# Kernel optimization log

Measured on AMD Instinct MI355X. Metric: run time of the kernel, lower is better.

The kernel has to match this reference:

```python
import jax, jax.numpy as jnp
import numpy as np

NEG_SLOPE = 0.2
EPS = 1e-16

N_NODES = 50000
N_EDGES = 800000
IN_C = 256
HID_C = 64
HEADS = 4
OUT_C = 128
N_GRAPHS = 100


def setup_inputs() -> dict:
    key = jax.random.key(0)
    ks = jax.random.split(key, 12)
    x = jax.random.normal(ks[0], (N_NODES, IN_C), dtype=jnp.float32)
    edge_index = jax.random.randint(ks[1], (2, N_EDGES), 0, N_NODES, dtype=jnp.int64)
    batch = jnp.sort(jax.random.randint(ks[2], (N_NODES,), 0, N_GRAPHS, dtype=jnp.int64))
    s1 = 1.0 / np.sqrt(IN_C)
    s2 = 1.0 / np.sqrt(HEADS * HID_C)
    W1 = jax.random.uniform(ks[3], (IN_C, HEADS * HID_C), jnp.float32, -s1, s1)
    att_src1 = jax.random.uniform(ks[4], (HEADS, HID_C), jnp.float32, -s1, s1)
    att_dst1 = jax.random.uniform(ks[5], (HEADS, HID_C), jnp.float32, -s1, s1)
    bias1 = jnp.zeros((HEADS * HID_C,), jnp.float32)
    W2 = jax.random.uniform(ks[6], (HEADS * HID_C, OUT_C), jnp.float32, -s2, s2)
    att_src2 = jax.random.uniform(ks[7], (1, OUT_C), jnp.float32, -s2, s2)
    att_dst2 = jax.random.uniform(ks[8], (1, OUT_C), jnp.float32, -s2, s2)
    bias2 = jnp.zeros((OUT_C,), jnp.float32)
    return {"x": x, "W1": W1, "att_src1": att_src1, "att_dst1": att_dst1,
            "bias1": bias1, "W2": W2, "att_src2": att_src2, "att_dst2": att_dst2,
            "bias2": bias2, "edge_index": edge_index, "batch": batch,
            "num_graphs": N_GRAPHS}


def gat_conv(x, W, att_src, att_dst, bias, src, dst, heads, ch):
    # x: [N, F_in]; W: [F_in, heads*ch]; att_*: [heads, ch]
    n = x.shape[0]
    h = (x @ W).reshape(n, heads, ch)                      # [N, H, C]
    a_src = jnp.sum(h * att_src[None], axis=-1)            # [N, H]
    a_dst = jnp.sum(h * att_dst[None], axis=-1)            # [N, H]
    alpha = a_src[src] + a_dst[dst]                        # [E, H]
    alpha = jax.nn.leaky_relu(alpha, NEG_SLOPE)
    # segment softmax over destination nodes (every node has a self-loop)
    amax = jax.ops.segment_max(alpha, dst, num_segments=n)
    e = jnp.exp(alpha - amax[dst])
    denom = jax.ops.segment_sum(e, dst, num_segments=n)
    alpha = e / (denom[dst] + EPS)                         # [E, H]
    msg = h[src] * alpha[:, :, None]                       # [E, H, C]
    out = jax.ops.segment_sum(msg, dst, num_segments=n)    # [N, H, C]
    return out.reshape(n, heads * ch) + bias


def reference(x, W1, att_src1, att_dst1, bias1, W2, att_src2, att_dst2, bias2,
              edge_index, batch, num_graphs):
    n = x.shape[0]
    loops = jnp.arange(n, dtype=edge_index.dtype)
    src = jnp.concatenate([edge_index[0], loops])
    dst = jnp.concatenate([edge_index[1], loops])
    h = gat_conv(x, W1, att_src1, att_dst1, bias1, src, dst, HEADS, HID_C)
    h = jax.nn.relu(h)
    h = gat_conv(h, W2, att_src2, att_dst2, bias2, src, dst, 1, OUT_C)
    h = jax.nn.relu(h)
    # global mean pool over graphs
    sums = jax.ops.segment_sum(h, batch, num_segments=num_graphs)
    cnt = jax.ops.segment_sum(jnp.ones((n, 1), h.dtype), batch, num_segments=num_graphs)
    return sums / jnp.maximum(cnt, 1.0)
```

## Files before the change

kernel.cpp:

```cpp
#include <hip/hip_runtime.h>
#include <hip/hip_bf16.h>
#include <hip/hip_fp16.h>

#define N_NODES 50000
#define N_EDGES 800000
#define E_TOT   (N_EDGES + N_NODES)
#define IN_C    256
#define H1C     256
#define HEADS   4
#define HID_C   64
#define OUT_C   128
#define N_GRAPHS 100
#define NEG_SLOPE 0.2f
#define EPS_F 1e-16f
#define SCAN_BLOCKS 196

#define NBUCKET 391
#define SORT_BLOCKS 104
#define EDGES_PER_SB 8192
#define BH_STRIDE 392
#define STAGE_CAP 3072

#define PREP_CAST_BLOCKS   12500
#define PREP_W1_BLOCKS     256
#define PREP_W2_BLOCKS     128
#define PREP_HIST_BLOCKS   3321
#define PREP_BOUNDS_BLOCKS 196
#define PREP_DOUT_BLOCKS   50
#define PREP_TOTAL (PREP_CAST_BLOCKS + PREP_W1_BLOCKS + PREP_W2_BLOCKS + PREP_HIST_BLOCKS + PREP_BOUNDS_BLOCKS + PREP_DOUT_BLOCKS)

typedef _Float16 half8_t __attribute__((ext_vector_type(8)));
typedef float f32x4 __attribute__((ext_vector_type(4)));

__global__ __launch_bounds__(256) void prep_kernel(const float* __restrict__ x,
                                                   _Float16* __restrict__ xh,
                                                   const float* __restrict__ W1,
                                                   _Float16* __restrict__ W1t,
                                                   const float* __restrict__ W2,
                                                   _Float16* __restrict__ W2t,
                                                   const int* __restrict__ ei,
                                                   int* __restrict__ hist,
                                                   const int* __restrict__ batch,
                                                   int* __restrict__ gstart,
                                                   float* __restrict__ d_out) {
    int b = blockIdx.x;
    int tid = threadIdx.x;
    if (b < PREP_CAST_BLOCKS) {
        int idx = b * 256 + tid;
        float4 v = reinterpret_cast<const float4*>(x)[idx];
        union { _Float16 h[4]; uint2 u; } p;
        p.h[0] = (_Float16)v.x; p.h[1] = (_Float16)v.y;
        p.h[2] = (_Float16)v.z; p.h[3] = (_Float16)v.w;
        reinterpret_cast<uint2*>(xh)[idx] = p.u;
        return;
    }
    b -= PREP_CAST_BLOCKS;
    if (b < PREP_W1_BLOCKS) {
        int idx = b * 256 + tid;
        int n = idx >> 8, k = idx & 255;
        W1t[idx] = (_Float16)W1[k * 256 + n];
        return;
    }
    b -= PREP_W1_BLOCKS;
    if (b < PREP_W2_BLOCKS) {
        int idx = b * 256 + tid;
        int n = idx >> 8, k = idx & 255;
        W2t[idx] = (_Float16)W2[k * 128 + n];
        return;
    }
    b -= PREP_W2_BLOCKS;
    if (b < PREP_HIST_BLOCKS) {
        int idx = b * 256 + tid;
        if (idx < N_EDGES) {
            int d = ei[N_EDGES + idx];
            if (d >= 0 && d < N_NODES) atomicAdd(&hist[d], 1);
        } else if (idx < E_TOT) {
            atomicAdd(&hist[idx - N_EDGES], 1);
        }
        return;
    }
    b -= PREP_HIST_BLOCKS;
    if (b < PREP_BOUNDS_BLOCKS) {
        int idx = b * 256 + tid;
        if (idx >= N_NODES) return;
        int g = batch[idx];
        if (g < 0) g = 0; if (g >= N_GRAPHS) g = N_GRAPHS - 1;
        if (idx == 0) {
            for (int j = 0; j <= g; ++j) gstart[j] = 0;
        } else {
            int gp = batch[idx - 1];
            if (gp < 0) gp = 0; if (gp >= N_GRAPHS) gp = N_GRAPHS - 1;
            for (int j = gp + 1; j <= g; ++j) gstart[j] = idx;
        }
        if (idx == N_NODES - 1) {
            for (int j = g + 1; j <= N_GRAPHS; ++j) gstart[j] = N_NODES;
        }
        return;
    }
    b -= PREP_BOUNDS_BLOCKS;
    {
        int idx = b * 256 + tid;
        if (idx < N_GRAPHS * 128) d_out[idx] = 0.f;
    }
}

__global__ __launch_bounds__(256) void scan_phase1(const int* __restrict__ hist,
                                                   int* __restrict__ blockSums) {
    __shared__ int lds[256];
    int idx = blockIdx.x * 256 + threadIdx.x;
    int v = (idx < N_NODES) ? hist[idx] : 0;
    lds[threadIdx.x] = v;
    __syncthreads();
#pragma unroll
    for (int off = 128; off > 0; off >>= 1) {
        if (threadIdx.x < off) lds[threadIdx.x] += lds[threadIdx.x + off];
        __syncthreads();
    }
    if (threadIdx.x == 0) blockSums[blockIdx.x] = lds[0];
}

__global__ __launch_bounds__(256) void scan_phase3(const int* __restrict__ hist,
                                                   const int* __restrict__ blockSums,
                                                   int* __restrict__ row_ptr) {
    __shared__ int lds[256];
    __shared__ int s_off;
    int b = blockIdx.x;
    int t = threadIdx.x;
    if (t < 64) {
        int acc = 0;
        for (int i = t; i < b; i += 64) acc += blockSums[i];
#pragma unroll
        for (int off = 32; off > 0; off >>= 1) acc += __shfl_down(acc, off);
        if (t == 0) s_off = acc;
    }
    int idx = b * 256 + t;
    int v = (idx < N_NODES) ? hist[idx] : 0;
    lds[t] = v;
    __syncthreads();
#pragma unroll
    for (int off = 1; off < 256; off <<= 1) {
        int u = (t >= off) ? lds[t - off] : 0;
        __syncthreads();
        lds[t] += u;
        __syncthreads();
    }
    int excl = lds[t] - v + s_off;
    if (idx < N_NODES) row_ptr[idx] = excl;
    if (idx == N_NODES - 1) row_ptr[N_NODES] = excl + v;
}

__global__ __launch_bounds__(256) void bucket_hist(const int* __restrict__ ei,
                                                   int* __restrict__ bhist) {
    __shared__ int bh[NBUCKET];
    int tid = threadIdx.x;
    for (int t = tid; t < NBUCKET; t += 256) bh[t] = 0;
    __syncthreads();
    int base = blockIdx.x * EDGES_PER_SB;
#pragma unroll 4
    for (int k = 0; k < EDGES_PER_SB / 256; ++k) {
        int idx = base + k * 256 + tid;
        int d = -1;
        if (idx < N_EDGES) d = ei[N_EDGES + idx];
        else if (idx < E_TOT) d = idx - N_EDGES;
        if (d >= 0 && d < N_NODES) atomicAdd(&bh[d >> 7], 1);
    }
    __syncthreads();
    for (int t = tid; t < NBUCKET; t += 256)
        bhist[blockIdx.x * BH_STRIDE + t] = bh[t];
}

__global__ __launch_bounds__(64) void bucket_scan(int* __restrict__ bhist) {
    int j = blockIdx.x;
    int lane = threadIdx.x;
    int carry = 0;
    for (int b0 = 0; b0 < SORT_BLOCKS; b0 += 64) {
        int b = b0 + lane;
        int v = (b < SORT_BLOCKS) ? bhist[b * BH_STRIDE + j] : 0;
        int inc = v;
#pragma unroll
        for (int off = 1; off < 64; off <<= 1) {
            int u = __shfl_up(inc, off);
            if (lane >= off) inc += u;
        }
        if (b < SORT_BLOCKS) bhist[b * BH_STRIDE + j] = inc - v + carry;
        carry += __shfl(inc, 63);
    }
}

__global__ __launch_bounds__(256) void bucket_bin(const int* __restrict__ ei,
                                                  const int* __restrict__ row_ptr,
                                                  const int* __restrict__ bhist,
                                                  int* __restrict__ ebuf) {
    __shared__ int cur[NBUCKET];
    int tid = threadIdx.x;
    for (int t = tid; t < NBUCKET; t += 256)
        cur[t] = row_ptr[t << 7] + bhist[blockIdx.x * BH_STRIDE + t];
    __syncthreads();
    int base = blockIdx.x * EDGES_PER_SB;
#pragma unroll 4
    for (int k = 0; k < EDGES_PER_SB / 256; ++k) {
        int idx = base + k * 256 + tid;
        int s = 0, d = -1;
        if (idx < N_EDGES) { s = ei[idx]; d = ei[N_EDGES + idx]; }
        else if (idx < E_TOT) { s = idx - N_EDGES; d = s; }
        if (d >= 0 && d < N_NODES) {
            int p = atomicAdd(&cur[d >> 7], 1);
            ebuf[p] = (s & 0xFFFF) | ((d & 127) << 16);
        }
    }
}

__global__ __launch_bounds__(256) void bucket_sort(const int* __restrict__ row_ptr,
                                                   const int* __restrict__ ebuf,
                                                   int* __restrict__ ssrc) {
    __shared__ int cur2[128];
    __shared__ int stage[STAGE_CAP];
    int j = blockIdx.x;
    int tid = threadIdx.x;
    int jn0 = j << 7;
    int nEnd = jn0 + 128; if (nEnd > N_NODES) nEnd = N_NODES;
    int lo = row_ptr[jn0];
    int hi = row_ptr[nEnd];
    int span = hi - lo;
    if (tid < nEnd - jn0) cur2[tid] = row_ptr[jn0 + tid] - lo;
    __syncthreads();
    if (span <= STAGE_CAP) {
        for (int t = lo + tid; t < hi; t += 256) {
            int v = ebuf[t];
            int p = atomicAdd(&cur2[v >> 16], 1);
            stage[p] = v & 0xFFFF;
        }
        __syncthreads();
        for (int t = tid; t < span; t += 256) ssrc[lo + t] = stage[t];
    } else {
        for (int t = lo + tid; t < hi; t += 256) {
            int v = ebuf[t];
            int p = atomicAdd(&cur2[v >> 16], 1);
            ssrc[lo + p] = v & 0xFFFF;
        }
    }
}

__global__ __launch_bounds__(256) void gemm_mfma_kernel(const _Float16* __restrict__ A,
                                                        const _Float16* __restrict__ Bt,
                                                        _Float16* __restrict__ C,
                                                        int mode,
                                                        const float* __restrict__ attS,
                                                        const float* __restrict__ attD,
                                                        float* __restrict__ a_src_o,
                                                        float* __restrict__ a_dst_o,
                                                        int M, int N) {
    __shared__ _Float16 As[128][48];
    __shared__ _Float16 Bs[128][48];
    __shared__ float lds_ps[128];
    __shared__ float lds_pd[128];
    const int tid = threadIdx.x;
    const int tileM = blockIdx.x * 128;
    const int tileN = blockIdx.y * 128;
    const int w = tid >> 6, lane = tid & 63;
    const int wm = (w >> 1) * 64, wn = (w & 1) * 64;
    const int quad = lane >> 4, mlane = lane & 15;
    const int srow = tid >> 2;
    const int schunk = (tid & 3) * 8;

    f32x4 zero = {0.f, 0.f, 0.f, 0.f};
    f32x4 acc[4][4];
#pragma unroll
    for (int i = 0; i < 4; ++i)
#pragma unroll
        for (int j = 0; j < 4; ++j) acc[i][j] = zero;

    const uint4* Av = reinterpret_cast<const uint4*>(A);
    const uint4* Bv = reinterpret_cast<const uint4*>(Bt);
    const int r0 = tileM + srow, r1 = r0 + 64;
    const bool ok0 = r0 < M, ok1 = r1 < M;
    const int bn0 = tileN + srow, bn1 = bn0 + 64;
    const uint4 z4 = make_uint4(0, 0, 0, 0);

    for (int k0 = 0; k0 < 256; k0 += 32) {
        const int kc = (k0 >> 3) + (tid & 3);
        uint4 a0 = ok0 ? Av[(size_t)r0 * 32 + kc] : z4;
        uint4 a1 = ok1 ? Av[(size_t)r1 * 32 + kc] : z4;
        uint4 b0 = Bv[(size_t)bn0 * 32 + kc];
        uint4 b1 = Bv[(size_t)bn1 * 32 + kc];
        __syncthreads();
        *reinterpret_cast<uint4*>(&As[srow][schunk]) = a0;
        *reinterpret_cast<uint4*>(&As[srow + 64][schunk]) = a1;
        *reinterpret_cast<uint4*>(&Bs[srow][schunk]) = b0;
        *reinterpret_cast<uint4*>(&Bs[srow + 64][schunk]) = b1;
        __syncthreads();
        half8_t af[4], bf[4];
#pragma unroll
        for (int mt = 0; mt < 4; ++mt)
            af[mt] = *reinterpret_cast<const half8_t*>(&As[wm + mt * 16 + mlane][quad * 8]);
#pragma unroll
        for (int nt = 0; nt < 4; ++nt)
            bf[nt] = *reinterpret_cast<const half8_t*>(&Bs[wn + nt * 16 + mlane][quad * 8]);
#pragma unroll
        for (int mt = 0; mt < 4; ++mt)
#pragma unroll
            for (int nt = 0; nt < 4; ++nt)
                acc[mt][nt] = __builtin_amdgcn_mfma_f32_16x16x32_f16(af[mt], bf[nt], acc[mt][nt], 0, 0, 0);
    }
#pragma unroll
    for (int mt = 0; mt < 4; ++mt) {
#pragma unroll
        for (int i = 0; i < 4; ++i) {
            int row = tileM + wm + mt * 16 + quad * 4 + i;
            if (row < M) {
                _Float16* cp = C + (size_t)row * N + tileN + wn;
#pragma unroll
                for (int nt = 0; nt < 4; ++nt)
                    cp[nt * 16 + mlane] = (_Float16)acc[mt][nt][i];
            }
        }
    }
    if (mode == 1) {
        int hd = (tileN + wn) >> 6;
        float as[4], ad[4];
#pragma unroll
        for (int nt = 0; nt < 4; ++nt) {
            as[nt] = attS[hd * 64 + nt * 16 + mlane];
            ad[nt] = attD[hd * 64 + nt * 16 + mlane];
        }
#pragma unroll
        for (int mt = 0; mt < 4; ++mt) {
#pragma unroll
            for (int i = 0; i < 4; ++i) {
                float ps = acc[mt][0][i] * as[0] + acc[mt][1][i] * as[1]
                         + acc[mt][2][i] * as[2] + acc[mt][3][i] * as[3];
                float pd = acc[mt][0][i] * ad[0] + acc[mt][1][i] * ad[1]
                         + acc[mt][2][i] * ad[2] + acc[mt][3][i] * ad[3];
#pragma unroll
                for (int off = 1; off < 16; off <<= 1) {
                    ps += __shfl_xor(ps, off);
                    pd += __shfl_xor(pd, off);
                }
                if (mlane == 0) {
                    int row = tileM + wm + mt * 16 + quad * 4 + i;
                    if (row < M) {
                        a_src_o[row * 4 + hd] = ps;
                        a_dst_o[row * 4 + hd] = pd;
                    }
                }
            }
        }
    } else if (mode == 2) {
        float as[4], ad[4];
#pragma unroll
        for (int nt = 0; nt < 4; ++nt) {
            as[nt] = attS[wn + nt * 16 + mlane];
            ad[nt] = attD[wn + nt * 16 + mlane];
        }
        float psa[4][4], pda[4][4];
#pragma unroll
        for (int mt = 0; mt < 4; ++mt) {
#pragma unroll
            for (int i = 0; i < 4; ++i) {
                float ps = acc[mt][0][i] * as[0] + acc[mt][1][i] * as[1]
                         + acc[mt][2][i] * as[2] + acc[mt][3][i] * as[3];
                float pd = acc[mt][0][i] * ad[0] + acc[mt][1][i] * ad[1]
                         + acc[mt][2][i] * ad[2] + acc[mt][3][i] * ad[3];
#pragma unroll
                for (int off = 1; off < 16; off <<= 1) {
                    ps += __shfl_xor(ps, off);
                    pd += __shfl_xor(pd, off);
                }
                psa[mt][i] = ps; pda[mt][i] = pd;
            }
        }
        __syncthreads();
        if (wn == 0 && mlane == 0) {
#pragma unroll
            for (int mt = 0; mt < 4; ++mt)
#pragma unroll
                for (int i = 0; i < 4; ++i) {
                    int lr = wm + mt * 16 + quad * 4 + i;
                    lds_ps[lr] = psa[mt][i];
                    lds_pd[lr] = pda[mt][i];
                }
        }
        __syncthreads();
        if (wn == 64 && mlane == 0) {
#pragma unroll
            for (int mt = 0; mt < 4; ++mt)
#pragma unroll
                for (int i = 0; i < 4; ++i) {
                    int lr = wm + mt * 16 + quad * 4 + i;
                    int row = tileM + lr;
                    if (row < M) {
                        a_src_o[row] = psa[mt][i] + lds_ps[lr];
                        a_dst_o[row] = pda[mt][i] + lds_pd[lr];
                    }
                }
        }
    }
}

__device__ __forceinline__ float lrelu(float x) { return x > 0.f ? x : NEG_SLOPE * x; }

__global__ __launch_bounds__(256) void edge1_kernel(const int* __restrict__ row_ptr,
                                                    const int* __restrict__ ssrc,
                                                    const __half* __restrict__ h1h,
                                                    const float* __restrict__ a_src,
                                                    const float* __restrict__ a_dst,
                                                    const float* __restrict__ bias,
                                                    __half* __restrict__ out) {
    int node = blockIdx.x * 4 + (threadIdx.x >> 6);
    int lane = threadIdx.x & 63;
    int hf   = lane >> 5;
    int cl   = lane & 31;
    int hd   = cl >> 3;
    int start = row_ptr[node], end = row_ptr[node + 1];
    int em1 = end - 1;
    float adh = a_dst[node * 4 + hd];

    const uint4* h1v = reinterpret_cast<const uint4*>(h1h);
    float4 aA0 = make_float4(0.f,0.f,0.f,0.f), aA1 = make_float4(0.f,0.f,0.f,0.f);
    float4 aB0 = make_float4(0.f,0.f,0.f,0.f), aB1 = make_float4(0.f,0.f,0.f,0.f);
    float s = 0.f;
    for (int e = start; e < end; e += 4) {
        int e0 = e + hf;
        int e1 = e + 2 + hf;
        int i0 = ssrc[e0 <= em1 ? e0 : em1];
        int i1 = ssrc[e1 <= em1 ? e1 : em1];
        float r0 = a_src[i0 * 4 + hd];
        float r1 = a_src[i1 * 4 + hd];
        uint4 q0 = h1v[(size_t)i0 * 32 + cl];
        uint4 q1 = h1v[(size_t)i1 * 32 + cl];
        float w0 = (e0 < end) ? __expf(lrelu(r0 + adh)) : 0.f;
        float w1 = (e1 < end) ? __expf(lrelu(r1 + adh)) : 0.f;
        s += w0 + w1;
        float2 f;
        f = __half22float2(*reinterpret_cast<const __half2*>(&q0.x)); aA0.x += w0*f.x; aA0.y += w0*f.y;
        f = __half22float2(*reinterpret_cast<const __half2*>(&q0.y)); aA0.z += w0*f.x; aA0.w += w0*f.y;
        f = __half22float2(*reinterpret_cast<const __half2*>(&q0.z)); aA1.x += w0*f.x; aA1.y += w0*f.y;
        f = __half22float2(*reinterpret_cast<const __half2*>(&q0.w)); aA1.z += w0*f.x; aA1.w += w0*f.y;
        f = __half22float2(*reinterpret_cast<const __half2*>(&q1.x)); aB0.x += w1*f.x; aB0.y += w1*f.y;
        f = __half22float2(*reinterpret_cast<const __half2*>(&q1.y)); aB0.z += w1*f.x; aB0.w += w1*f.y;
        f = __half22float2(*reinterpret_cast<const __half2*>(&q1.z)); aB1.x += w1*f.x; aB1.y += w1*f.y;
        f = __half22float2(*reinterpret_cast<const __half2*>(&q1.w)); aB1.z += w1*f.x; aB1.w += w1*f.y;
    }
    float4 c0, c1;
    c0.x = aA0.x + aB0.x; c0.y = aA0.y + aB0.y; c0.z = aA0.z + aB0.z; c0.w = aA0.w + aB0.w;
    c1.x = aA1.x + aB1.x; c1.y = aA1.y + aB1.y; c1.z = aA1.z + aB1.z; c1.w = aA1.w + aB1.w;
    c0.x += __shfl_xor(c0.x, 32); c0.y += __shfl_xor(c0.y, 32);
    c0.z += __shfl_xor(c0.z, 32); c0.w += __shfl_xor(c0.w, 32);
    c1.x += __shfl_xor(c1.x, 32); c1.y += __shfl_xor(c1.y, 32);
    c1.z += __shfl_xor(c1.z, 32); c1.w += __shfl_xor(c1.w, 32);
    s += __shfl_xor(s, 32);
    float inv = 1.0f / (s + EPS_F);
    if (lane < 32) {
        const float4* b4 = reinterpret_cast<const float4*>(bias);
        float4 b0 = b4[cl * 2], b1 = b4[cl * 2 + 1];
        union { _Float16 h[8]; uint4 u; } st;
        st.h[0] = (_Float16)fmaxf(c0.x * inv + b0.x, 0.f);
        st.h[1] = (_Float16)fmaxf(c0.y * inv + b0.y, 0.f);
        st.h[2] = (_Float16)fmaxf(c0.z * inv + b0.z, 0.f);
        st.h[3] = (_Float16)fmaxf(c0.w * inv + b0.w, 0.f);
        st.h[4] = (_Float16)fmaxf(c1.x * inv + b1.x, 0.f);
        st.h[5] = (_Float16)fmaxf(c1.y * inv + b1.y, 0.f);
        st.h[6] = (_Float16)fmaxf(c1.z * inv + b1.z, 0.f);
        st.h[7] = (_Float16)fmaxf(c1.w * inv + b1.w, 0.f);
        reinterpret_cast<uint4*>(out)[(size_t)node * 32 + cl] = st.u;
    }
}

__global__ __launch_bounds__(256) void edge2_kernel(const int* __restrict__ row_ptr,
                                                    const int* __restrict__ ssrc,
                                                    const __half* __restrict__ h2h,
                                                    const float* __restrict__ a_src,
                                                    const float* __restrict__ a_dst,
                                                    const float* __restrict__ bias,
                                                    float* __restrict__ out) {
    int lane = threadIdx.x & 63;
    int node = blockIdx.x * 8 + ((threadIdx.x >> 6) << 1) + (lane >> 5);
    int sub  = (lane >> 4) & 1;
    int cl   = lane & 15;
    int start = row_ptr[node], end = row_ptr[node + 1];
    int em1 = end - 1;
    float ad = a_dst[node];

    const uint4* h2v = reinterpret_cast<const uint4*>(h2h);
    float4 aA0 = make_float4(0.f,0.f,0.f,0.f), aA1 = make_float4(0.f,0.f,0.f,0.f);
    float4 aB0 = make_float4(0.f,0.f,0.f,0.f), aB1 = make_float4(0.f,0.f,0.f,0.f);
    float s = 0.f;
    for (int e = start; e < end; e += 4) {
        int e0 = e + sub;
        int e1 = e + 2 + sub;
        int i0 = ssrc[e0 <= em1 ? e0 : em1];
        int i1 = ssrc[e1 <= em1 ? e1 : em1];
        float r0 = a_src[i0];
        float r1 = a_src[i1];
        uint4 q0 = h2v[(size_t)i0 * 16 + cl];
        uint4 q1 = h2v[(size_t)i1 * 16 + cl];
        float w0 = (e0 < end) ? __expf(lrelu(r0 + ad)) : 0.f;
        float w1 = (e1 < end) ? __expf(lrelu(r1 + ad)) : 0.f;
        s += w0 + w1;
        float2 f;
        f = __half22float2(*reinterpret_cast<const __half2*>(&q0.x)); aA0.x += w0*f.x; aA0.y += w0*f.y;
        f = __half22float2(*reinterpret_cast<const __half2*>(&q0.y)); aA0.z += w0*f.x; aA0.w += w0*f.y;
        f = __half22float2(*reinterpret_cast<const __half2*>(&q0.z)); aA1.x += w0*f.x; aA1.y += w0*f.y;
        f = __half22float2(*reinterpret_cast<const __half2*>(&q0.w)); aA1.z += w0*f.x; aA1.w += w0*f.y;
        f = __half22float2(*reinterpret_cast<const __half2*>(&q1.x)); aB0.x += w1*f.x; aB0.y += w1*f.y;
        f = __half22float2(*reinterpret_cast<const __half2*>(&q1.y)); aB0.z += w1*f.x; aB0.w += w1*f.y;
        f = __half22float2(*reinterpret_cast<const __half2*>(&q1.z)); aB1.x += w1*f.x; aB1.y += w1*f.y;
        f = __half22float2(*reinterpret_cast<const __half2*>(&q1.w)); aB1.z += w1*f.x; aB1.w += w1*f.y;
    }
    float4 c0, c1;
    c0.x = aA0.x + aB0.x; c0.y = aA0.y + aB0.y; c0.z = aA0.z + aB0.z; c0.w = aA0.w + aB0.w;
    c1.x = aA1.x + aB1.x; c1.y = aA1.y + aB1.y; c1.z = aA1.z + aB1.z; c1.w = aA1.w + aB1.w;
    c0.x += __shfl_xor(c0.x, 16); c0.y += __shfl_xor(c0.y, 16);
    c0.z += __shfl_xor(c0.z, 16); c0.w += __shfl_xor(c0.w, 16);
    c1.x += __shfl_xor(c1.x, 16); c1.y += __shfl_xor(c1.y, 16);
    c1.z += __shfl_xor(c1.z, 16); c1.w += __shfl_xor(c1.w, 16);
    s += __shfl_xor(s, 16);
    float inv = 1.0f / (s + EPS_F);
    if (sub == 0) {
        const float4* b4 = reinterpret_cast<const float4*>(bias);
        float4 b0 = b4[cl * 2], b1 = b4[cl * 2 + 1];
        float4 o0, o1;
        o0.x = fmaxf(c0.x * inv + b0.x, 0.f);
        o0.y = fmaxf(c0.y * inv + b0.y, 0.f);
        o0.z = fmaxf(c0.z * inv + b0.z, 0.f);
        o0.w = fmaxf(c0.w * inv + b0.w, 0.f);
        o1.x = fmaxf(c1.x * inv + b1.x, 0.f);
        o1.y = fmaxf(c1.y * inv + b1.y, 0.f);
        o1.z = fmaxf(c1.z * inv + b1.z, 0.f);
        o1.w = fmaxf(c1.w * inv + b1.w, 0.f);
        float4* o4 = reinterpret_cast<float4*>(out) + (size_t)node * 32 + cl * 2;
        o4[0] = o0;
        o4[1] = o1;
    }
}

#define POOL_CHUNK 64
__global__ __launch_bounds__(128) void pool_kernel(const float* __restrict__ out2,
                                                   const int* __restrict__ batch,
                                                   const int* __restrict__ gstart,
                                                   float* __restrict__ d_out) {
    int c = threadIdx.x;
    int node0 = blockIdx.x * POOL_CHUNK;
    int nodeEnd = node0 + POOL_CHUNK; if (nodeEnd > N_NODES) nodeEnd = N_NODES;
    if (node0 >= N_NODES) return;
    int gprev = batch[node0];
    float acc = 0.f;
    for (int node = node0; node < nodeEnd; ++node) {
        int g = batch[node];
        if (g != gprev) {
            if (gprev >= 0 && gprev < N_GRAPHS) {
                float cnt = (float)(gstart[gprev + 1] - gstart[gprev]);
                if (cnt < 1.f) cnt = 1.f;
                atomicAdd(&d_out[gprev * 128 + c], acc / cnt);
            }
            acc = 0.f;
            gprev = g;
        }
        acc += out2[(size_t)node * 128 + c];
    }
    if (gprev >= 0 && gprev < N_GRAPHS) {
        float cnt = (float)(gstart[gprev + 1] - gstart[gprev]);
        if (cnt < 1.f) cnt = 1.f;
        atomicAdd(&d_out[gprev * 128 + c], acc / cnt);
    }
}

extern "C" void kernel_launch(void* const* d_in, const int* in_sizes, int n_in,
                              void* d_out_v, int out_size, void* d_ws, size_t ws_size,
                              hipStream_t stream) {
    const float* x      = (const float*)d_in[0];
    const float* W1     = (const float*)d_in[1];
    const float* att_s1 = (const float*)d_in[2];
    const float* att_d1 = (const float*)d_in[3];
    const float* bias1  = (const float*)d_in[4];
    const float* W2     = (const float*)d_in[5];
    const float* att_s2 = (const float*)d_in[6];
    const float* att_d2 = (const float*)d_in[7];
    const float* bias2  = (const float*)d_in[8];
    const int*   ei     = (const int*)d_in[9];
    const int*   batch  = (const int*)d_in[10];
    float* d_out = (float*)d_out_v;

    float* ws = (float*)d_ws;
    _Float16* xh    = (_Float16*)ws;
    _Float16* h1h   = (_Float16*)(ws + 6400000);
    _Float16* out1h = (_Float16*)(ws + 12800000);
    _Float16* h2h   = (_Float16*)ws;
    float*    out2  = ws + 6400000;
    float* a_src1 = ws + 19200000;
    float* a_dst1 = a_src1 + 200000;
    float* a_src2 = a_dst1 + 200000;
    float* a_dst2 = a_src2 + 50000;
    int* hist     = (int*)(a_dst2 + 50000);
    int* row_ptr  = hist + 50000;
    int* ssrc     = row_ptr + 50016;
    int* ebuf     = ssrc + 850000;
    int* bhist    = ebuf + 851968;
    int* gstart   = bhist + (SORT_BLOCKS * BH_STRIDE);
    int* blockSums = gstart + 128;
    _Float16* W1t = (_Float16*)(blockSums + 256);
    _Float16* W2t = W1t + 65536;

    hipMemsetAsync(hist, 0, N_NODES * sizeof(int), stream);

    prep_kernel<<<PREP_TOTAL, 256, 0, stream>>>(x, xh, W1, W1t, W2, W2t,
                                                ei, hist, batch, gstart, d_out);

    scan_phase1<<<SCAN_BLOCKS, 256, 0, stream>>>(hist, blockSums);
    scan_phase3<<<SCAN_BLOCKS, 256, 0, stream>>>(hist, blockSums, row_ptr);

    bucket_hist<<<SORT_BLOCKS, 256, 0, stream>>>(ei, bhist);
    bucket_scan<<<NBUCKET, 64, 0, stream>>>(bhist);
    bucket_bin<<<SORT_BLOCKS, 256, 0, stream>>>(ei, row_ptr, bhist, ebuf);
    bucket_sort<<<NBUCKET, 256, 0, stream>>>(row_ptr, ebuf, ssrc);

    {
        dim3 g((N_NODES + 127) / 128, H1C / 128);
        gemm_mfma_kernel<<<g, 256, 0, stream>>>(xh, W1t, h1h, 1,
                                                att_s1, att_d1, a_src1, a_dst1,
                                                N_NODES, H1C);
    }
    edge1_kernel<<<N_NODES / 4, 256, 0, stream>>>(row_ptr, ssrc, (const __half*)h1h,
                                                  a_src1, a_dst1, bias1, (__half*)out1h);

    {
        dim3 g((N_NODES + 127) / 128, OUT_C / 128);
        gemm_mfma_kernel<<<g, 256, 0, stream>>>(out1h, W2t, h2h, 2,
                                                att_s2, att_d2, a_src2, a_dst2,
                                                N_NODES, OUT_C);
    }
    edge2_kernel<<<N_NODES / 8, 256, 0, stream>>>(row_ptr, ssrc, (const __half*)h2h,
                                                  a_src2, a_dst2, bias2, out2);

    pool_kernel<<<(N_NODES + POOL_CHUNK - 1) / POOL_CHUNK, 128, 0, stream>>>(out2, batch, gstart, d_out);
}
```

Baseline: 345.6 us.

## Software-pipeline neighbor gathers in GAT aggregation and repad GEMM LDS tiles

Both aggregation kernels now prefetch the next group's feature rows and attention scalars, and the index after that, one iteration ahead. This lets gather latency overlap with the current accumulation instead of serialising index, then feature loads, then math. The GEMM LDS tile row stride grows from 48 to 56 halves to change the bank-conflict pattern. The prefetch adds register pressure and an extra index load per iteration, and the new padding raises LDS use per block.

```diff
diff --git a/kernel.cpp b/kernel.cpp
--- a/kernel.cpp
+++ b/kernel.cpp
@@ -250,8 +250,8 @@
                                                         float* __restrict__ a_src_o,
                                                         float* __restrict__ a_dst_o,
                                                         int M, int N) {
-    __shared__ _Float16 As[128][48];
-    __shared__ _Float16 Bs[128][48];
+    __shared__ _Float16 As[128][56];
+    __shared__ _Float16 Bs[128][56];
     __shared__ float lds_ps[128];
     __shared__ float lds_pd[128];
     const int tid = threadIdx.x;
@@ -419,17 +419,31 @@
     float4 aA0 = make_float4(0.f,0.f,0.f,0.f), aA1 = make_float4(0.f,0.f,0.f,0.f);
     float4 aB0 = make_float4(0.f,0.f,0.f,0.f), aB1 = make_float4(0.f,0.f,0.f,0.f);
     float s = 0.f;
+
+    int e0 = start + hf, e1 = start + 2 + hf;
+    int i0 = ssrc[e0 <= em1 ? e0 : em1];
+    int i1 = ssrc[e1 <= em1 ? e1 : em1];
+    uint4 q0 = h1v[(size_t)i0 * 32 + cl];
+    uint4 q1 = h1v[(size_t)i1 * 32 + cl];
+    float r0 = a_src[i0 * 4 + hd];
+    float r1 = a_src[i1 * 4 + hd];
+    int f0 = start + 4 + hf, f1 = start + 6 + hf;
+    int j0 = ssrc[f0 <= em1 ? f0 : em1];
+    int j1 = ssrc[f1 <= em1 ? f1 : em1];
+
     for (int e = start; e < end; e += 4) {
-        int e0 = e + hf;
-        int e1 = e + 2 + hf;
-        int i0 = ssrc[e0 <= em1 ? e0 : em1];
-        int i1 = ssrc[e1 <= em1 ? e1 : em1];
-        float r0 = a_src[i0 * 4 + hd];
-        float r1 = a_src[i1 * 4 + hd];
-        uint4 q0 = h1v[(size_t)i0 * 32 + cl];
-        uint4 q1 = h1v[(size_t)i1 * 32 + cl];
-        float w0 = (e0 < end) ? __expf(lrelu(r0 + adh)) : 0.f;
-        float w1 = (e1 < end) ? __expf(lrelu(r1 + adh)) : 0.f;
+        uint4 p0, p1; float t0, t1;
+        if (e + 4 < end) {
+            p0 = h1v[(size_t)j0 * 32 + cl];
+            p1 = h1v[(size_t)j1 * 32 + cl];
+            t0 = a_src[j0 * 4 + hd];
+            t1 = a_src[j1 * 4 + hd];
+        }
+        int g0 = e + 8 + hf, g1 = e + 10 + hf;
+        int k0 = ssrc[g0 <= em1 ? g0 : em1];
+        int k1 = ssrc[g1 <= em1 ? g1 : em1];
+        float w0 = (e + hf < end)     ? __expf(lrelu(r0 + adh)) : 0.f;
+        float w1 = (e + 2 + hf < end) ? __expf(lrelu(r1 + adh)) : 0.f;
         s += w0 + w1;
         float2 f;
         f = __half22float2(*reinterpret_cast<const __half2*>(&q0.x)); aA0.x += w0*f.x; aA0.y += w0*f.y;
@@ -440,6 +454,7 @@
         f = __half22float2(*reinterpret_cast<const __half2*>(&q1.y)); aB0.z += w1*f.x; aB0.w += w1*f.y;
         f = __half22float2(*reinterpret_cast<const __half2*>(&q1.z)); aB1.x += w1*f.x; aB1.y += w1*f.y;
         f = __half22float2(*reinterpret_cast<const __half2*>(&q1.w)); aB1.z += w1*f.x; aB1.w += w1*f.y;
+        q0 = p0; q1 = p1; r0 = t0; r1 = t1; j0 = k0; j1 = k1;
     }
     float4 c0, c1;
     c0.x = aA0.x + aB0.x; c0.y = aA0.y + aB0.y; c0.z = aA0.z + aB0.z; c0.w = aA0.w + aB0.w;
@@ -485,17 +500,31 @@
     float4 aA0 = make_float4(0.f,0.f,0.f,0.f), aA1 = make_float4(0.f,0.f,0.f,0.f);
     float4 aB0 = make_float4(0.f,0.f,0.f,0.f), aB1 = make_float4(0.f,0.f,0.f,0.f);
     float s = 0.f;
+
+    int e0 = start + sub, e1 = start + 2 + sub;
+    int i0 = ssrc[e0 <= em1 ? e0 : em1];
+    int i1 = ssrc[e1 <= em1 ? e1 : em1];
+    uint4 q0 = h2v[(size_t)i0 * 16 + cl];
+    uint4 q1 = h2v[(size_t)i1 * 16 + cl];
+    float r0 = a_src[i0];
+    float r1 = a_src[i1];
+    int f0 = start + 4 + sub, f1 = start + 6 + sub;
+    int j0 = ssrc[f0 <= em1 ? f0 : em1];
+    int j1 = ssrc[f1 <= em1 ? f1 : em1];
+
     for (int e = start; e < end; e += 4) {
-        int e0 = e + sub;
-        int e1 = e + 2 + sub;
-        int i0 = ssrc[e0 <= em1 ? e0 : em1];
-        int i1 = ssrc[e1 <= em1 ? e1 : em1];
-        float r0 = a_src[i0];
-        float r1 = a_src[i1];
-        uint4 q0 = h2v[(size_t)i0 * 16 + cl];
-        uint4 q1 = h2v[(size_t)i1 * 16 + cl];
-        float w0 = (e0 < end) ? __expf(lrelu(r0 + ad)) : 0.f;
-        float w1 = (e1 < end) ? __expf(lrelu(r1 + ad)) : 0.f;
+        uint4 p0, p1; float t0, t1;
+        if (e + 4 < end) {
+            p0 = h2v[(size_t)j0 * 16 + cl];
+            p1 = h2v[(size_t)j1 * 16 + cl];
+            t0 = a_src[j0];
+            t1 = a_src[j1];
+        }
+        int g0 = e + 8 + sub, g1 = e + 10 + sub;
+        int k0 = ssrc[g0 <= em1 ? g0 : em1];
+        int k1 = ssrc[g1 <= em1 ? g1 : em1];
+        float w0 = (e + sub < end)     ? __expf(lrelu(r0 + ad)) : 0.f;
+        float w1 = (e + 2 + sub < end) ? __expf(lrelu(r1 + ad)) : 0.f;
         s += w0 + w1;
         float2 f;
         f = __half22float2(*reinterpret_cast<const __half2*>(&q0.x)); aA0.x += w0*f.x; aA0.y += w0*f.y;
@@ -506,6 +535,7 @@
         f = __half22float2(*reinterpret_cast<const __half2*>(&q1.y)); aB0.z += w1*f.x; aB0.w += w1*f.y;
         f = __half22float2(*reinterpret_cast<const __half2*>(&q1.z)); aB1.x += w1*f.x; aB1.y += w1*f.y;
         f = __half22float2(*reinterpret_cast<const __half2*>(&q1.w)); aB1.z += w1*f.x; aB1.w += w1*f.y;
+        q0 = p0; q1 = p1; r0 = t0; r1 = t1; j0 = k0; j1 = k1;
     }
     float4 c0, c1;
     c0.x = aA0.x + aB0.x; c0.y = aA0.y + aB0.y; c0.z = aA0.z + aB0.z; c0.w = aA0.w + aB0.w;
```

New measurement: 346.8 us. No clear change (+0.3%).

## Derive CSR row pointers inside bucket sort and drop global degree histogram

Applied to the files above, without the earlier changes.

Removes the per-node global atomic histogram, the memset and the two-kernel scan. Bucket totals are now scanned in a small single-block kernel, and each bucket_sort block counts its own per-node degrees in LDS to write row_ptr. The bucket histogram moves into the prep kernel, so two launches and 850k global atomics disappear, at the cost of an extra pass over ebuf in bucket_sort. The GEMM LDS tile padding also changes from 48 to 56 columns, which alters the bank-conflict pattern.

```diff
diff --git a/kernel.cpp b/kernel.cpp
--- a/kernel.cpp
+++ b/kernel.cpp
@@ -13,7 +13,6 @@
 #define N_GRAPHS 100
 #define NEG_SLOPE 0.2f
 #define EPS_F 1e-16f
-#define SCAN_BLOCKS 196
 
 #define NBUCKET 391
 #define SORT_BLOCKS 104
@@ -21,13 +20,13 @@
 #define BH_STRIDE 392
 #define STAGE_CAP 3072
 
+#define PREP_BHIST_BLOCKS  104
 #define PREP_CAST_BLOCKS   12500
 #define PREP_W1_BLOCKS     256
 #define PREP_W2_BLOCKS     128
-#define PREP_HIST_BLOCKS   3321
 #define PREP_BOUNDS_BLOCKS 196
 #define PREP_DOUT_BLOCKS   50
-#define PREP_TOTAL (PREP_CAST_BLOCKS + PREP_W1_BLOCKS + PREP_W2_BLOCKS + PREP_HIST_BLOCKS + PREP_BOUNDS_BLOCKS + PREP_DOUT_BLOCKS)
+#define PREP_TOTAL (PREP_BHIST_BLOCKS + PREP_CAST_BLOCKS + PREP_W1_BLOCKS + PREP_W2_BLOCKS + PREP_BOUNDS_BLOCKS + PREP_DOUT_BLOCKS)
 
 typedef _Float16 half8_t __attribute__((ext_vector_type(8)));
 typedef float f32x4 __attribute__((ext_vector_type(4)));
@@ -39,12 +38,31 @@
                                                    const float* __restrict__ W2,
                                                    _Float16* __restrict__ W2t,
                                                    const int* __restrict__ ei,
-                                                   int* __restrict__ hist,
+                                                   int* __restrict__ bhist,
                                                    const int* __restrict__ batch,
                                                    int* __restrict__ gstart,
                                                    float* __restrict__ d_out) {
+    __shared__ int bh[NBUCKET];
     int b = blockIdx.x;
     int tid = threadIdx.x;
+    if (b < PREP_BHIST_BLOCKS) {
+        for (int t = tid; t < NBUCKET; t += 256) bh[t] = 0;
+        __syncthreads();
+        int base = b * EDGES_PER_SB;
+#pragma unroll 4
+        for (int k = 0; k < EDGES_PER_SB / 256; ++k) {
+            int idx = base + k * 256 + tid;
+            int d = -1;
+            if (idx < N_EDGES) d = ei[N_EDGES + idx];
+            else if (idx < E_TOT) d = idx - N_EDGES;
+            if (d >= 0 && d < N_NODES) atomicAdd(&bh[d >> 7], 1);
+        }
+        __syncthreads();
+        for (int t = tid; t < NBUCKET; t += 256)
+            bhist[b * BH_STRIDE + t] = bh[t];
+        return;
+    }
+    b -= PREP_BHIST_BLOCKS;
     if (b < PREP_CAST_BLOCKS) {
         int idx = b * 256 + tid;
         float4 v = reinterpret_cast<const float4*>(x)[idx];
@@ -69,17 +87,6 @@
         return;
     }
     b -= PREP_W2_BLOCKS;
-    if (b < PREP_HIST_BLOCKS) {
-        int idx = b * 256 + tid;
-        if (idx < N_EDGES) {
-            int d = ei[N_EDGES + idx];
-            if (d >= 0 && d < N_NODES) atomicAdd(&hist[d], 1);
-        } else if (idx < E_TOT) {
-            atomicAdd(&hist[idx - N_EDGES], 1);
-        }
-        return;
-    }
-    b -= PREP_HIST_BLOCKS;
     if (b < PREP_BOUNDS_BLOCKS) {
         int idx = b * 256 + tid;
         if (idx >= N_NODES) return;
@@ -104,72 +111,8 @@
     }
 }
 
-__global__ __launch_bounds__(256) void scan_phase1(const int* __restrict__ hist,
-                                                   int* __restrict__ blockSums) {
-    __shared__ int lds[256];
-    int idx = blockIdx.x * 256 + threadIdx.x;
-    int v = (idx < N_NODES) ? hist[idx] : 0;
-    lds[threadIdx.x] = v;
-    __syncthreads();
-#pragma unroll
-    for (int off = 128; off > 0; off >>= 1) {
-        if (threadIdx.x < off) lds[threadIdx.x] += lds[threadIdx.x + off];
-        __syncthreads();
-    }
-    if (threadIdx.x == 0) blockSums[blockIdx.x] = lds[0];
-}
-
-__global__ __launch_bounds__(256) void scan_phase3(const int* __restrict__ hist,
-                                                   const int* __restrict__ blockSums,
-                                                   int* __restrict__ row_ptr) {
-    __shared__ int lds[256];
-    __shared__ int s_off;
-    int b = blockIdx.x;
-    int t = threadIdx.x;
-    if (t < 64) {
-        int acc = 0;
-        for (int i = t; i < b; i += 64) acc += blockSums[i];
-#pragma unroll
-        for (int off = 32; off > 0; off >>= 1) acc += __shfl_down(acc, off);
-        if (t == 0) s_off = acc;
-    }
-    int idx = b * 256 + t;
-    int v = (idx < N_NODES) ? hist[idx] : 0;
-    lds[t] = v;
-    __syncthreads();
-#pragma unroll
-    for (int off = 1; off < 256; off <<= 1) {
-        int u = (t >= off) ? lds[t - off] : 0;
-        __syncthreads();
-        lds[t] += u;
-        __syncthreads();
-    }
-    int excl = lds[t] - v + s_off;
-    if (idx < N_NODES) row_ptr[idx] = excl;
-    if (idx == N_NODES - 1) row_ptr[N_NODES] = excl + v;
-}
-
-__global__ __launch_bounds__(256) void bucket_hist(const int* __restrict__ ei,
-                                                   int* __restrict__ bhist) {
-    __shared__ int bh[NBUCKET];
-    int tid = threadIdx.x;
-    for (int t = tid; t < NBUCKET; t += 256) bh[t] = 0;
-    __syncthreads();
-    int base = blockIdx.x * EDGES_PER_SB;
-#pragma unroll 4
-    for (int k = 0; k < EDGES_PER_SB / 256; ++k) {
-        int idx = base + k * 256 + tid;
-        int d = -1;
-        if (idx < N_EDGES) d = ei[N_EDGES + idx];
-        else if (idx < E_TOT) d = idx - N_EDGES;
-        if (d >= 0 && d < N_NODES) atomicAdd(&bh[d >> 7], 1);
-    }
-    __syncthreads();
-    for (int t = tid; t < NBUCKET; t += 256)
-        bhist[blockIdx.x * BH_STRIDE + t] = bh[t];
-}
-
-__global__ __launch_bounds__(64) void bucket_scan(int* __restrict__ bhist) {
+__global__ __launch_bounds__(64) void bucket_scan(int* __restrict__ bhist,
+                                                  int* __restrict__ btot) {
     int j = blockIdx.x;
     int lane = threadIdx.x;
     int carry = 0;
@@ -185,16 +128,35 @@
         if (b < SORT_BLOCKS) bhist[b * BH_STRIDE + j] = inc - v + carry;
         carry += __shfl(inc, 63);
     }
+    if (lane == 0) btot[j] = carry;
+}
+
+__global__ __launch_bounds__(512) void bucket_base(const int* __restrict__ btot,
+                                                   int* __restrict__ bbase) {
+    __shared__ int lds[512];
+    int t = threadIdx.x;
+    int v = (t < NBUCKET) ? btot[t] : 0;
+    lds[t] = v;
+    __syncthreads();
+#pragma unroll
+    for (int off = 1; off < 512; off <<= 1) {
+        int u = (t >= off) ? lds[t - off] : 0;
+        __syncthreads();
+        lds[t] += u;
+        __syncthreads();
+    }
+    if (t < NBUCKET) bbase[t] = lds[t] - v;
+    if (t == NBUCKET - 1) bbase[NBUCKET] = lds[t];
 }
 
 __global__ __launch_bounds__(256) void bucket_bin(const int* __restrict__ ei,
-                                                  const int* __restrict__ row_ptr,
+                                                  const int* __restrict__ bbase,
                                                   const int* __restrict__ bhist,
                                                   int* __restrict__ ebuf) {
     __shared__ int cur[NBUCKET];
     int tid = threadIdx.x;
     for (int t = tid; t < NBUCKET; t += 256)
-        cur[t] = row_ptr[t << 7] + bhist[blockIdx.x * BH_STRIDE + t];
+        cur[t] = bbase[t] + bhist[blockIdx.x * BH_STRIDE + t];
     __syncthreads();
     int base = blockIdx.x * EDGES_PER_SB;
 #pragma unroll 4
@@ -210,24 +172,45 @@
     }
 }
 
-__global__ __launch_bounds__(256) void bucket_sort(const int* __restrict__ row_ptr,
+__global__ __launch_bounds__(256) void bucket_sort(const int* __restrict__ bbase,
                                                    const int* __restrict__ ebuf,
-                                                   int* __restrict__ ssrc) {
-    __shared__ int cur2[128];
+                                                   int* __restrict__ ssrc,
+                                                   int* __restrict__ row_ptr) {
+    __shared__ int cnt[128];
+    __shared__ int sc[128];
     __shared__ int stage[STAGE_CAP];
     int j = blockIdx.x;
     int tid = threadIdx.x;
     int jn0 = j << 7;
-    int nEnd = jn0 + 128; if (nEnd > N_NODES) nEnd = N_NODES;
-    int lo = row_ptr[jn0];
-    int hi = row_ptr[nEnd];
+    int nNodes = N_NODES - jn0; if (nNodes > 128) nNodes = 128;
+    int lo = bbase[j];
+    int hi = bbase[j + 1];
     int span = hi - lo;
-    if (tid < nEnd - jn0) cur2[tid] = row_ptr[jn0 + tid] - lo;
+    if (tid < 128) cnt[tid] = 0;
+    __syncthreads();
+    for (int t = lo + tid; t < hi; t += 256)
+        atomicAdd(&cnt[(ebuf[t] >> 16) & 127], 1);
+    __syncthreads();
+    if (tid < 128) sc[tid] = cnt[tid];
+    __syncthreads();
+#pragma unroll
+    for (int off = 1; off < 128; off <<= 1) {
+        int u = (tid >= off && tid < 128) ? sc[tid - off] : 0;
+        __syncthreads();
+        if (tid < 128) sc[tid] += u;
+        __syncthreads();
+    }
+    if (tid < 128) {
+        int excl = sc[tid] - cnt[tid];
+        if (tid < nNodes) row_ptr[jn0 + tid] = lo + excl;
+        cnt[tid] = excl;
+    }
+    if (j == NBUCKET - 1 && tid == 0) row_ptr[N_NODES] = hi;
     __syncthreads();
     if (span <= STAGE_CAP) {
         for (int t = lo + tid; t < hi; t += 256) {
             int v = ebuf[t];
-            int p = atomicAdd(&cur2[v >> 16], 1);
+            int p = atomicAdd(&cnt[(v >> 16) & 127], 1);
             stage[p] = v & 0xFFFF;
         }
         __syncthreads();
@@ -235,8 +218,8 @@
     } else {
         for (int t = lo + tid; t < hi; t += 256) {
             int v = ebuf[t];
-            int p = atomicAdd(&cur2[v >> 16], 1);
-            ssrc[lo + p] = v & 0xFFFF;
+            int p = atomicAdd(&cnt[(v >> 16) & 127], 1);
+            if (p >= 0 && p < span) ssrc[lo + p] = v & 0xFFFF;
         }
     }
 }
@@ -250,8 +233,8 @@
                                                         float* __restrict__ a_src_o,
                                                         float* __restrict__ a_dst_o,
                                                         int M, int N) {
-    __shared__ _Float16 As[128][48];
-    __shared__ _Float16 Bs[128][48];
+    __shared__ _Float16 As[128][56];
+    __shared__ _Float16 Bs[128][56];
     __shared__ float lds_ps[128];
     __shared__ float lds_pd[128];
     const int tid = threadIdx.x;
@@ -591,28 +574,23 @@
     float* a_dst1 = a_src1 + 200000;
     float* a_src2 = a_dst1 + 200000;
     float* a_dst2 = a_src2 + 50000;
-    int* hist     = (int*)(a_dst2 + 50000);
-    int* row_ptr  = hist + 50000;
+    int* row_ptr  = (int*)(a_dst2 + 50000);
     int* ssrc     = row_ptr + 50016;
     int* ebuf     = ssrc + 850000;
     int* bhist    = ebuf + 851968;
-    int* gstart   = bhist + (SORT_BLOCKS * BH_STRIDE);
-    int* blockSums = gstart + 128;
-    _Float16* W1t = (_Float16*)(blockSums + 256);
+    int* btot     = bhist + (SORT_BLOCKS * BH_STRIDE);
+    int* bbase    = btot + 512;
+    int* gstart   = bbase + 512;
+    _Float16* W1t = (_Float16*)(gstart + 128);
     _Float16* W2t = W1t + 65536;
 
-    hipMemsetAsync(hist, 0, N_NODES * sizeof(int), stream);
-
     prep_kernel<<<PREP_TOTAL, 256, 0, stream>>>(x, xh, W1, W1t, W2, W2t,
-                                                ei, hist, batch, gstart, d_out);
-
-    scan_phase1<<<SCAN_BLOCKS, 256, 0, stream>>>(hist, blockSums);
-    scan_phase3<<<SCAN_BLOCKS, 256, 0, stream>>>(hist, blockSums, row_ptr);
-
-    bucket_hist<<<SORT_BLOCKS, 256, 0, stream>>>(ei, bhist);
-    bucket_scan<<<NBUCKET, 64, 0, stream>>>(bhist);
-    bucket_bin<<<SORT_BLOCKS, 256, 0, stream>>>(ei, row_ptr, bhist, ebuf);
-    bucket_sort<<<NBUCKET, 256, 0, stream>>>(row_ptr, ebuf, ssrc);
+                                                ei, bhist, batch, gstart, d_out);
+
+    bucket_scan<<<NBUCKET, 64, 0, stream>>>(bhist, btot);
+    bucket_base<<<1, 512, 0, stream>>>(btot, bbase);
+    bucket_bin<<<SORT_BLOCKS, 256, 0, stream>>>(ei, bbase, bhist, ebuf);
+    bucket_sort<<<NBUCKET, 256, 0, stream>>>(bbase, ebuf, ssrc, row_ptr);
 
     {
         dim3 g((N_NODES + 127) / 128, H1C / 128);
```

Result: faster. 302.2 us (-12.6%).
